# Optimization experiments

Hardware: AMD Instinct MI355X
Metric: run time of the kernel (lower is better)

The kernel has to match this reference:

```python
import jax, jax.numpy as jnp
import numpy as np

HEADS = 8
EMBED = 512


def setup_inputs() -> dict:
    key = jax.random.key(0)
    ks = jax.random.split(key, 9)
    N, KL, QL, S = 4, 512, 32, 64
    D = EMBED // HEADS
    return {
        "values": jax.random.normal(ks[0], (N, KL, EMBED), jnp.float32),
        "keys": jax.random.normal(ks[1], (N, KL, EMBED), jnp.float32),
        "query": jax.random.normal(ks[2], (N, QL, S, EMBED), jnp.float32),
        "mask": jax.random.randint(ks[3], (N, 1, 1, KL, 1), 0, 2, jnp.int32),
        "Wv": jax.random.normal(ks[4], (D, D), jnp.float32) * 0.05,
        "Wk": jax.random.normal(ks[5], (D, D), jnp.float32) * 0.05,
        "Wq": jax.random.normal(ks[6], (D, D), jnp.float32) * 0.05,
        "Wo": jax.random.normal(ks[7], (EMBED, EMBED), jnp.float32) * 0.05,
        "bo": jax.random.normal(ks[8], (EMBED,), jnp.float32) * 0.05,
    }


def reference(values, keys, query, mask, Wv, Wk, Wq, Wo, bo):
    N, KL, E = keys.shape
    QL, S = query.shape[1], query.shape[2]
    H = HEADS
    D = E // H
    # split heads, then per-head linear (weights shared across heads, torch y = x @ W.T)
    v = jnp.einsum('nkhd,ed->nkhe', values.reshape(N, KL, H, D), Wv)
    k = jnp.einsum('nkhd,ed->nkhe', keys.reshape(N, KL, H, D), Wk)
    q = jnp.einsum('nqshd,ed->nqshe', query.reshape(N, QL, S, H, D), Wq)
    # energy: [N, H, QL, KL, S]
    energy = jnp.einsum('nqshd,nkhd->nhqks', q, k)
    energy = jnp.where(mask == 0, jnp.float32(-1e20), energy)
    scale = jnp.float32(E ** 0.5)
    attention = jax.nn.softmax(energy / scale, axis=3)  # softmax over key axis
    out = jnp.einsum('nhqks,nkhd->nqshd', attention, v).reshape(N, QL, S, E)
    return out @ Wo.T + bo
```

## Files before the change

### kernel.cpp

```cpp
#include <hip/hip_runtime.h>
#include <math.h>


typedef __bf16 bf16;
typedef __attribute__((ext_vector_type(8))) __bf16 bf16x8;
typedef __attribute__((ext_vector_type(4))) __bf16 bf16x4;
typedef __attribute__((ext_vector_type(4))) float f32x4;

#define LW 68
#define LS 72
#define QSCALE (0.044194173824159216f * 1.4426950408889634f)
#define MASK_BIAS -64.0f

__device__ __forceinline__ bf16x8 cvt8(const float* p, float s) {
    float4 x0 = *(const float4*)p;
    float4 x1 = *(const float4*)(p + 4);
    return (bf16x8){(bf16)(x0.x * s), (bf16)(x0.y * s), (bf16)(x0.z * s), (bf16)(x0.w * s),
                    (bf16)(x1.x * s), (bf16)(x1.y * s), (bf16)(x1.z * s), (bf16)(x1.w * s)};
}

__global__ __launch_bounds__(256, 2) void kv_proj(const float* __restrict__ keys,
                                                  const float* __restrict__ values,
                                                  const float* __restrict__ Wk,
                                                  const float* __restrict__ Wv,
                                                  bf16* __restrict__ Kp,
                                                  bf16* __restrict__ Vt) {
    __shared__ bf16 Xk[32 * LW];
    __shared__ bf16 Xv[32 * LW];
    int t = threadIdx.x;
    int nh = blockIdx.x >> 4, klt = blockIdx.x & 15;
    int n = nh >> 3, h = nh & 7, kl0 = klt * 32;
    int w = t >> 6, quad = (t >> 4) & 3, c16 = t & 15;
#pragma unroll
    for (int i = 0; i < 2; ++i) {
        int f = t + i * 256, row = f >> 4, c4 = f & 15;
        float4 a = *(const float4*)(keys + ((long)n * 512 + kl0 + row) * 512 + h * 64 + c4 * 4);
        float4 b = *(const float4*)(values + ((long)n * 512 + kl0 + row) * 512 + h * 64 + c4 * 4);
        *(bf16x4*)&Xk[row * LW + c4 * 4] = (bf16x4){(bf16)a.x, (bf16)a.y, (bf16)a.z, (bf16)a.w};
        *(bf16x4*)&Xv[row * LW + c4 * 4] = (bf16x4){(bf16)b.x, (bf16)b.y, (bf16)b.z, (bf16)b.w};
    }
    __syncthreads();
    if (w < 2) {
        f32x4 acc[4];
#pragma unroll
        for (int nb = 0; nb < 4; ++nb) acc[nb] = (f32x4){0.f, 0.f, 0.f, 0.f};
#pragma unroll
        for (int kc = 0; kc < 2; ++kc) {
            bf16x8 a = *(const bf16x8*)&Xk[(16 * w + c16) * LW + 32 * kc + quad * 8];
#pragma unroll
            for (int nb = 0; nb < 4; ++nb) {
                bf16x8 b = cvt8(Wk + (16 * nb + c16) * 64 + 32 * kc + quad * 8, 1.0f);
                acc[nb] = __builtin_amdgcn_mfma_f32_16x16x32_bf16(a, b, acc[nb], 0, 0, 0);
            }
        }
#pragma unroll
        for (int nb = 0; nb < 4; ++nb)
#pragma unroll
            for (int r = 0; r < 4; ++r)
                Kp[((long)nh * 512 + kl0 + 16 * w + quad * 4 + r) * 64 + 16 * nb + c16] =
                    (bf16)acc[nb][r];
    } else {
        int w2 = w - 2;
        f32x4 acc[2][2];
#pragma unroll
        for (int mb = 0; mb < 2; ++mb)
#pragma unroll
            for (int nb = 0; nb < 2; ++nb) acc[mb][nb] = (f32x4){0.f, 0.f, 0.f, 0.f};
#pragma unroll
        for (int kc = 0; kc < 2; ++kc) {
#pragma unroll
            for (int mb = 0; mb < 2; ++mb) {
                bf16x8 a = cvt8(Wv + (32 * w2 + 16 * mb + c16) * 64 + 32 * kc + quad * 8, 1.0f);
#pragma unroll
                for (int nb = 0; nb < 2; ++nb) {
                    bf16x8 b = *(const bf16x8*)&Xv[(16 * nb + c16) * LW + 32 * kc + quad * 8];
                    acc[mb][nb] = __builtin_amdgcn_mfma_f32_16x16x32_bf16(a, b, acc[mb][nb], 0, 0, 0);
                }
            }
        }
#pragma unroll
        for (int mb = 0; mb < 2; ++mb)
#pragma unroll
            for (int nb = 0; nb < 2; ++nb)
#pragma unroll
                for (int r = 0; r < 4; ++r)
                    Vt[((long)nh * 64 + 32 * w2 + 16 * mb + quad * 4 + r) * 512 + kl0 + 16 * nb + c16] =
                        (bf16)acc[mb][nb][r];
    }
}

__global__ __launch_bounds__(256, 4) void attn(const float* __restrict__ query,
                                               const float* __restrict__ Wq,
                                               const bf16* __restrict__ Kp,
                                               const bf16* __restrict__ Vtg,
                                               const int* __restrict__ maskp,
                                               bf16* __restrict__ AOp,
                                               float* __restrict__ Lb) {
    __shared__ bf16 SX[64 * LS];
    __shared__ bf16 Kt[64 * LW];
    __shared__ bf16 Vs[64 * LW];
    int t = threadIdx.x;
    int nh = blockIdx.x & 31, half = (blockIdx.x >> 5) & 1, qtile = blockIdx.x >> 6;
    int n = nh >> 3, h = nh & 7;
    int r0 = qtile * 64;
    int kt0 = half * 4;
    int w = t >> 6, quad = (t >> 4) & 3, c16 = t & 15;
    const bf16* Kb = Kp + (long)nh * 512 * 64;
    const bf16* Vb = Vtg + (long)nh * 64 * 512;

    int prow0 = t >> 3, pcol0 = t & 7;
    int prow1 = (t + 256) >> 3, pcol1 = t & 7;
    bf16x8 pk0 = *(const bf16x8*)(Kb + (long)(kt0 * 64 + prow0) * 64 + pcol0 * 8);
    bf16x8 pk1 = *(const bf16x8*)(Kb + (long)(kt0 * 64 + prow1) * 64 + pcol1 * 8);
    bf16x8 pv0 = *(const bf16x8*)(Vb + (long)prow0 * 512 + kt0 * 64 + pcol0 * 8);
    bf16x8 pv1 = *(const bf16x8*)(Vb + (long)prow1 * 512 + kt0 * 64 + pcol1 * 8);

    bf16x8 wf[8];
#pragma unroll
    for (int nb = 0; nb < 4; ++nb)
#pragma unroll
        for (int kc = 0; kc < 2; ++kc)
            wf[nb * 2 + kc] = cvt8(Wq + (16 * nb + c16) * 64 + 32 * kc + quad * 8, QSCALE);

    {
        int l = t & 63;
        int rloc = 16 * w + (l >> 2);
        const float* qrow = query + ((long)n * 2048 + r0 + rloc) * 512 + h * 64;
#pragma unroll
        for (int j = 0; j < 4; ++j) {
            int c = (l & 3) + 4 * j;
            float4 a = *(const float4*)(qrow + c * 4);
            *(bf16x4*)&SX[rloc * LS + c * 4] = (bf16x4){(bf16)a.x, (bf16)a.y, (bf16)a.z, (bf16)a.w};
        }
    }
    f32x4 qa[4];
#pragma unroll
    for (int nb = 0; nb < 4; ++nb) qa[nb] = (f32x4){0.f, 0.f, 0.f, 0.f};
#pragma unroll
    for (int kc = 0; kc < 2; ++kc) {
        bf16x8 a = *(const bf16x8*)&SX[(16 * w + c16) * LS + 32 * kc + quad * 8];
#pragma unroll
        for (int nb = 0; nb < 4; ++nb)
            qa[nb] = __builtin_amdgcn_mfma_f32_16x16x32_bf16(a, wf[nb * 2 + kc], qa[nb], 0, 0, 0);
    }
#pragma unroll
    for (int nb = 0; nb < 4; ++nb)
#pragma unroll
        for (int r = 0; r < 4; ++r)
            SX[(16 * w + quad * 4 + r) * LS + 16 * nb + c16] = (bf16)qa[nb][r];
    bf16x8 qf[2];
#pragma unroll
    for (int kc = 0; kc < 2; ++kc)
        qf[kc] = *(const bf16x8*)&SX[(16 * w + c16) * LS + 32 * kc + quad * 8];

    f32x4 oacc[4];
#pragma unroll
    for (int mb = 0; mb < 4; ++mb) oacc[mb] = (f32x4){0.f, 0.f, 0.f, 0.f};
    float ps = 0.f;

    for (int kt = 0; kt < 4; ++kt) {
        int tk = kt0 + kt;
        if (kt) __syncthreads();
        *(bf16x8*)&Kt[prow0 * LW + pcol0 * 8] = pk0;
        *(bf16x8*)&Kt[prow1 * LW + pcol1 * 8] = pk1;
        *(bf16x8*)&Vs[prow0 * LW + pcol0 * 8] = pv0;
        *(bf16x8*)&Vs[prow1 * LW + pcol1 * 8] = pv1;
        __syncthreads();
        if (kt < 3) {
            pk0 = *(const bf16x8*)(Kb + (long)((tk + 1) * 64 + prow0) * 64 + pcol0 * 8);
            pk1 = *(const bf16x8*)(Kb + (long)((tk + 1) * 64 + prow1) * 64 + pcol1 * 8);
            pv0 = *(const bf16x8*)(Vb + (long)prow0 * 512 + (tk + 1) * 64 + pcol0 * 8);
            pv1 = *(const bf16x8*)(Vb + (long)prow1 * 512 + (tk + 1) * 64 + pcol1 * 8);
        }
        f32x4 sc[4];
#pragma unroll
        for (int mb = 0; mb < 4; ++mb) {
            int4 mk = *(const int4*)(maskp + n * 512 + tk * 64 + 16 * mb + quad * 4);
            sc[mb] = (f32x4){mk.x ? 0.f : MASK_BIAS, mk.y ? 0.f : MASK_BIAS,
                             mk.z ? 0.f : MASK_BIAS, mk.w ? 0.f : MASK_BIAS};
        }
#pragma unroll
        for (int kc = 0; kc < 2; ++kc) {
#pragma unroll
            for (int mb = 0; mb < 4; ++mb) {
                bf16x8 ka = *(const bf16x8*)&Kt[(16 * mb + c16) * LW + 32 * kc + quad * 8];
                sc[mb] = __builtin_amdgcn_mfma_f32_16x16x32_bf16(ka, qf[kc], sc[mb], 0, 0, 0);
            }
        }
#pragma unroll
        for (int mb = 0; mb < 4; ++mb) {
            float p0 = exp2f(sc[mb][0]);
            float p1 = exp2f(sc[mb][1]);
            float p2 = exp2f(sc[mb][2]);
            float p3 = exp2f(sc[mb][3]);
            ps += (p0 + p1) + (p2 + p3);
            *(bf16x4*)&SX[(16 * w + c16) * LS + 16 * mb + quad * 4] =
                (bf16x4){(bf16)p0, (bf16)p1, (bf16)p2, (bf16)p3};
        }
#pragma unroll
        for (int kc = 0; kc < 2; ++kc) {
            bf16x8 pb = *(const bf16x8*)&SX[(16 * w + c16) * LS + 32 * kc + quad * 8];
#pragma unroll
            for (int mb = 0; mb < 4; ++mb) {
                bf16x8 va = *(const bf16x8*)&Vs[(16 * mb + c16) * LW + 32 * kc + quad * 8];
                oacc[mb] = __builtin_amdgcn_mfma_f32_16x16x32_bf16(va, pb, oacc[mb], 0, 0, 0);
            }
        }
    }
    ps += __shfl_xor(ps, 16);
    ps += __shfl_xor(ps, 32);
    int row_g = r0 + 16 * w + c16;
    bf16* AO = AOp + (long)half * 4194304;
#pragma unroll
    for (int mb = 0; mb < 4; ++mb)
        *(bf16x4*)(AO + ((long)n * 2048 + row_g) * 512 + h * 64 + 16 * mb + quad * 4) =
            (bf16x4){(bf16)oacc[mb][0], (bf16)oacc[mb][1], (bf16)oacc[mb][2], (bf16)oacc[mb][3]};
    if (quad == 0) Lb[half * 65536 + nh * 2048 + row_g] = ps;
}

__global__ __launch_bounds__(256, 4) void out_gemm(const bf16* __restrict__ AOp,
                                                   const float* __restrict__ Lb,
                                                   const float* __restrict__ Wo,
                                                   const float* __restrict__ bo,
                                                   float* __restrict__ C) {
    __shared__ bf16 At[64 * LW];
    __shared__ bf16 Bt[64 * LW];
    int t = threadIdx.x;
    int br = blockIdx.x & 127, bc = blockIdx.x >> 7;
    int r0 = br * 64, c0 = bc * 64;
    int w = t >> 6, quad = (t >> 4) & 3, c16 = t & 15;
    const bf16* AO2 = AOp + 4194304;
    int arow[2], acol[2], wrow[4], wcol[4];
#pragma unroll
    for (int i = 0; i < 2; ++i) {
        int f = t + i * 256;
        arow[i] = f >> 3;
        acol[i] = f & 7;
    }
#pragma unroll
    for (int i = 0; i < 4; ++i) {
        int f = t + i * 256;
        wrow[i] = f >> 4;
        wcol[i] = f & 15;
    }
    bf16x8 pa1[2], pa2[2];
    float4 pw[4];
#pragma unroll
    for (int i = 0; i < 2; ++i) {
        pa1[i] = *(const bf16x8*)(AOp + (long)(r0 + arow[i]) * 512 + acol[i] * 8);
        pa2[i] = *(const bf16x8*)(AO2 + (long)(r0 + arow[i]) * 512 + acol[i] * 8);
    }
#pragma unroll
    for (int i = 0; i < 4; ++i)
        pw[i] = *(const float4*)(Wo + (long)(c0 + wrow[i]) * 512 + wcol[i] * 4);
    f32x4 acc[4];
#pragma unroll
    for (int nb = 0; nb < 4; ++nb) acc[nb] = (f32x4){0.f, 0.f, 0.f, 0.f};
    for (int k0 = 0; k0 < 512; k0 += 64) {
        int hh = k0 >> 6;
        if (k0) __syncthreads();
#pragma unroll
        for (int i = 0; i < 2; ++i) {
            int grow = r0 + arow[i];
            int lidx = ((grow >> 11) * 8 + hh) * 2048 + (grow & 2047);
            float il = 1.0f / (Lb[lidx] + Lb[65536 + lidx]);
            bf16x8 o;
#pragma unroll
            for (int e = 0; e < 8; ++e)
                o[e] = (bf16)(((float)pa1[i][e] + (float)pa2[i][e]) * il);
            *(bf16x8*)&At[arow[i] * LW + acol[i] * 8] = o;
        }
#pragma unroll
        for (int i = 0; i < 4; ++i)
            *(bf16x4*)&Bt[wrow[i] * LW + wcol[i] * 4] =
                (bf16x4){(bf16)pw[i].x, (bf16)pw[i].y, (bf16)pw[i].z, (bf16)pw[i].w};
        __syncthreads();
        if (k0 < 448) {
#pragma unroll
            for (int i = 0; i < 2; ++i) {
                pa1[i] = *(const bf16x8*)(AOp + (long)(r0 + arow[i]) * 512 + k0 + 64 + acol[i] * 8);
                pa2[i] = *(const bf16x8*)(AO2 + (long)(r0 + arow[i]) * 512 + k0 + 64 + acol[i] * 8);
            }
#pragma unroll
            for (int i = 0; i < 4; ++i)
                pw[i] = *(const float4*)(Wo + (long)(c0 + wrow[i]) * 512 + k0 + 64 + wcol[i] * 4);
        }
#pragma unroll
        for (int kc = 0; kc < 2; ++kc) {
            bf16x8 a = *(const bf16x8*)&At[(16 * w + c16) * LW + 32 * kc + quad * 8];
#pragma unroll
            for (int nb = 0; nb < 4; ++nb) {
                bf16x8 b = *(const bf16x8*)&Bt[(16 * nb + c16) * LW + 32 * kc + quad * 8];
                acc[nb] = __builtin_amdgcn_mfma_f32_16x16x32_bf16(a, b, acc[nb], 0, 0, 0);
            }
        }
    }
#pragma unroll
    for (int nb = 0; nb < 4; ++nb) {
        float bias = bo[c0 + 16 * nb + c16];
#pragma unroll
        for (int r = 0; r < 4; ++r)
            C[(long)(r0 + 16 * w + quad * 4 + r) * 512 + c0 + 16 * nb + c16] = acc[nb][r] + bias;
    }
}

extern "C" void kernel_launch(void* const* d_in, const int* in_sizes, int n_in,
                              void* d_out, int out_size, void* d_ws, size_t ws_size,
                              hipStream_t stream) {
    const float* values = (const float*)d_in[0];
    const float* keys   = (const float*)d_in[1];
    const float* query  = (const float*)d_in[2];
    const int*   maskp  = (const int*)d_in[3];
    const float* Wv     = (const float*)d_in[4];
    const float* Wk     = (const float*)d_in[5];
    const float* Wq     = (const float*)d_in[6];
    const float* Wo     = (const float*)d_in[7];
    const float* bo     = (const float*)d_in[8];
    float* out = (float*)d_out;

    bf16* ws = (bf16*)d_ws;
    bf16* Kp  = ws;
    bf16* Vt  = Kp + 1048576;
    bf16* AOp = Vt + 1048576;
    float* Lb = (float*)(AOp + 8388608);

    kv_proj<<<dim3(512), dim3(256), 0, stream>>>(keys, values, Wk, Wv, Kp, Vt);
    attn<<<dim3(2048), dim3(256), 0, stream>>>(query, Wq, Kp, Vt, maskp, AOp, Lb);
    out_gemm<<<dim3(1024), dim3(256), 0, stream>>>(AOp, Lb, Wo, bo, out);
}
```

Measured before the change: 144.2 us.

## Fuse attention with output projection, one 512-thread block per 16 rows

Merges the attention and output-GEMM kernels into a single kernel. Each 512-thread block handles 16 query rows across all 8 heads, one wave per head, and does not split the key length. The normalized attention output stays in shared memory and is multiplied directly by a bf16 copy of Wo, which the prep kernel now converts. This removes the global round-trip of the split partial outputs and row sums and one launch. In exchange, K and V fragments are read straight from global memory without LDS staging, and there are fewer, larger blocks.

New measurement: 187.2 us. 29.8% more time.

```diff
diff --git a/kernel.cpp b/kernel.cpp
--- a/kernel.cpp
+++ b/kernel.cpp
@@ -9,6 +9,7 @@
 
 #define LW 68
 #define LS 72
+#define AOW 524
 #define QSCALE (0.044194173824159216f * 1.4426950408889634f)
 #define MASK_BIAS -64.0f
 
@@ -19,15 +20,23 @@
                     (bf16)(x1.x * s), (bf16)(x1.y * s), (bf16)(x1.z * s), (bf16)(x1.w * s)};
 }
 
-__global__ __launch_bounds__(256, 2) void kv_proj(const float* __restrict__ keys,
-                                                  const float* __restrict__ values,
-                                                  const float* __restrict__ Wk,
-                                                  const float* __restrict__ Wv,
-                                                  bf16* __restrict__ Kp,
-                                                  bf16* __restrict__ Vt) {
+__global__ __launch_bounds__(256, 2) void prep(const float* __restrict__ keys,
+                                               const float* __restrict__ values,
+                                               const float* __restrict__ Wk,
+                                               const float* __restrict__ Wv,
+                                               const float* __restrict__ Wo,
+                                               bf16* __restrict__ Kp,
+                                               bf16* __restrict__ Vt,
+                                               bf16* __restrict__ Wo_bf) {
     __shared__ bf16 Xk[32 * LW];
     __shared__ bf16 Xv[32 * LW];
     int t = threadIdx.x;
+    if (blockIdx.x >= 512) {
+        int i0 = (blockIdx.x - 512) * 4096 + t * 16;
+        *(bf16x8*)(Wo_bf + i0) = cvt8(Wo + i0, 1.0f);
+        *(bf16x8*)(Wo_bf + i0 + 8) = cvt8(Wo + i0 + 8, 1.0f);
+        return;
+    }
     int nh = blockIdx.x >> 4, klt = blockIdx.x & 15;
     int n = nh >> 3, h = nh & 7, kl0 = klt * 32;
     int w = t >> 6, quad = (t >> 4) & 3, c16 = t & 15;
@@ -89,31 +98,24 @@
     }
 }
 
-__global__ __launch_bounds__(256, 4) void attn(const float* __restrict__ query,
-                                               const float* __restrict__ Wq,
-                                               const bf16* __restrict__ Kp,
-                                               const bf16* __restrict__ Vtg,
-                                               const int* __restrict__ maskp,
-                                               bf16* __restrict__ AOp,
-                                               float* __restrict__ Lb) {
-    __shared__ bf16 SX[64 * LS];
-    __shared__ bf16 Kt[64 * LW];
-    __shared__ bf16 Vs[64 * LW];
+__global__ __launch_bounds__(512, 4) void attn_gemm(const float* __restrict__ query,
+                                                    const float* __restrict__ Wq,
+                                                    const bf16* __restrict__ Kp,
+                                                    const bf16* __restrict__ Vtg,
+                                                    const int* __restrict__ maskp,
+                                                    const bf16* __restrict__ Wo_bf,
+                                                    const float* __restrict__ bo,
+                                                    float* __restrict__ out) {
+    __shared__ bf16 PW[128 * LS];
+    __shared__ bf16 AOt[16 * AOW];
     int t = threadIdx.x;
-    int nh = blockIdx.x & 31, half = (blockIdx.x >> 5) & 1, qtile = blockIdx.x >> 6;
-    int n = nh >> 3, h = nh & 7;
-    int r0 = qtile * 64;
-    int kt0 = half * 4;
     int w = t >> 6, quad = (t >> 4) & 3, c16 = t & 15;
+    int n = blockIdx.x >> 7, qt = blockIdx.x & 127;
+    int r0 = qt * 16;
+    int nh = n * 8 + w;
     const bf16* Kb = Kp + (long)nh * 512 * 64;
     const bf16* Vb = Vtg + (long)nh * 64 * 512;
-
-    int prow0 = t >> 3, pcol0 = t & 7;
-    int prow1 = (t + 256) >> 3, pcol1 = t & 7;
-    bf16x8 pk0 = *(const bf16x8*)(Kb + (long)(kt0 * 64 + prow0) * 64 + pcol0 * 8);
-    bf16x8 pk1 = *(const bf16x8*)(Kb + (long)(kt0 * 64 + prow1) * 64 + pcol1 * 8);
-    bf16x8 pv0 = *(const bf16x8*)(Vb + (long)prow0 * 512 + kt0 * 64 + pcol0 * 8);
-    bf16x8 pv1 = *(const bf16x8*)(Vb + (long)prow1 * 512 + kt0 * 64 + pcol1 * 8);
+    bf16* Pw = PW + w * 16 * LS;
 
     bf16x8 wf[8];
 #pragma unroll
@@ -124,13 +126,13 @@
 
     {
         int l = t & 63;
-        int rloc = 16 * w + (l >> 2);
-        const float* qrow = query + ((long)n * 2048 + r0 + rloc) * 512 + h * 64;
+        int rl = l >> 2;
+        const float* qrow = query + ((long)n * 2048 + r0 + rl) * 512 + w * 64;
 #pragma unroll
         for (int j = 0; j < 4; ++j) {
             int c = (l & 3) + 4 * j;
             float4 a = *(const float4*)(qrow + c * 4);
-            *(bf16x4*)&SX[rloc * LS + c * 4] = (bf16x4){(bf16)a.x, (bf16)a.y, (bf16)a.z, (bf16)a.w};
+            *(bf16x4*)&Pw[rl * LS + c * 4] = (bf16x4){(bf16)a.x, (bf16)a.y, (bf16)a.z, (bf16)a.w};
         }
     }
     f32x4 qa[4];
@@ -138,7 +140,7 @@
     for (int nb = 0; nb < 4; ++nb) qa[nb] = (f32x4){0.f, 0.f, 0.f, 0.f};
 #pragma unroll
     for (int kc = 0; kc < 2; ++kc) {
-        bf16x8 a = *(const bf16x8*)&SX[(16 * w + c16) * LS + 32 * kc + quad * 8];
+        bf16x8 a = *(const bf16x8*)&Pw[c16 * LS + 32 * kc + quad * 8];
 #pragma unroll
         for (int nb = 0; nb < 4; ++nb)
             qa[nb] = __builtin_amdgcn_mfma_f32_16x16x32_bf16(a, wf[nb * 2 + kc], qa[nb], 0, 0, 0);
@@ -147,35 +149,22 @@
     for (int nb = 0; nb < 4; ++nb)
 #pragma unroll
         for (int r = 0; r < 4; ++r)
-            SX[(16 * w + quad * 4 + r) * LS + 16 * nb + c16] = (bf16)qa[nb][r];
+            Pw[(quad * 4 + r) * LS + 16 * nb + c16] = (bf16)qa[nb][r];
     bf16x8 qf[2];
 #pragma unroll
     for (int kc = 0; kc < 2; ++kc)
-        qf[kc] = *(const bf16x8*)&SX[(16 * w + c16) * LS + 32 * kc + quad * 8];
+        qf[kc] = *(const bf16x8*)&Pw[c16 * LS + 32 * kc + quad * 8];
 
     f32x4 oacc[4];
 #pragma unroll
     for (int mb = 0; mb < 4; ++mb) oacc[mb] = (f32x4){0.f, 0.f, 0.f, 0.f};
     float ps = 0.f;
 
-    for (int kt = 0; kt < 4; ++kt) {
-        int tk = kt0 + kt;
-        if (kt) __syncthreads();
-        *(bf16x8*)&Kt[prow0 * LW + pcol0 * 8] = pk0;
-        *(bf16x8*)&Kt[prow1 * LW + pcol1 * 8] = pk1;
-        *(bf16x8*)&Vs[prow0 * LW + pcol0 * 8] = pv0;
-        *(bf16x8*)&Vs[prow1 * LW + pcol1 * 8] = pv1;
-        __syncthreads();
-        if (kt < 3) {
-            pk0 = *(const bf16x8*)(Kb + (long)((tk + 1) * 64 + prow0) * 64 + pcol0 * 8);
-            pk1 = *(const bf16x8*)(Kb + (long)((tk + 1) * 64 + prow1) * 64 + pcol1 * 8);
-            pv0 = *(const bf16x8*)(Vb + (long)prow0 * 512 + (tk + 1) * 64 + pcol0 * 8);
-            pv1 = *(const bf16x8*)(Vb + (long)prow1 * 512 + (tk + 1) * 64 + pcol1 * 8);
-        }
+    for (int kt = 0; kt < 8; ++kt) {
         f32x4 sc[4];
 #pragma unroll
         for (int mb = 0; mb < 4; ++mb) {
-            int4 mk = *(const int4*)(maskp + n * 512 + tk * 64 + 16 * mb + quad * 4);
+            int4 mk = *(const int4*)(maskp + n * 512 + kt * 64 + 16 * mb + quad * 4);
             sc[mb] = (f32x4){mk.x ? 0.f : MASK_BIAS, mk.y ? 0.f : MASK_BIAS,
                              mk.z ? 0.f : MASK_BIAS, mk.w ? 0.f : MASK_BIAS};
         }
@@ -183,7 +172,7 @@
         for (int kc = 0; kc < 2; ++kc) {
 #pragma unroll
             for (int mb = 0; mb < 4; ++mb) {
-                bf16x8 ka = *(const bf16x8*)&Kt[(16 * mb + c16) * LW + 32 * kc + quad * 8];
+                bf16x8 ka = *(const bf16x8*)(Kb + (long)(kt * 64 + 16 * mb + c16) * 64 + 32 * kc + quad * 8);
                 sc[mb] = __builtin_amdgcn_mfma_f32_16x16x32_bf16(ka, qf[kc], sc[mb], 0, 0, 0);
             }
         }
@@ -194,113 +183,48 @@
             float p2 = exp2f(sc[mb][2]);
             float p3 = exp2f(sc[mb][3]);
             ps += (p0 + p1) + (p2 + p3);
-            *(bf16x4*)&SX[(16 * w + c16) * LS + 16 * mb + quad * 4] =
+            *(bf16x4*)&Pw[c16 * LS + 16 * mb + quad * 4] =
                 (bf16x4){(bf16)p0, (bf16)p1, (bf16)p2, (bf16)p3};
         }
 #pragma unroll
         for (int kc = 0; kc < 2; ++kc) {
-            bf16x8 pb = *(const bf16x8*)&SX[(16 * w + c16) * LS + 32 * kc + quad * 8];
+            bf16x8 pb = *(const bf16x8*)&Pw[c16 * LS + 32 * kc + quad * 8];
 #pragma unroll
             for (int mb = 0; mb < 4; ++mb) {
-                bf16x8 va = *(const bf16x8*)&Vs[(16 * mb + c16) * LW + 32 * kc + quad * 8];
+                bf16x8 va = *(const bf16x8*)(Vb + (long)(16 * mb + c16) * 512 + kt * 64 + 32 * kc + quad * 8);
                 oacc[mb] = __builtin_amdgcn_mfma_f32_16x16x32_bf16(va, pb, oacc[mb], 0, 0, 0);
             }
         }
     }
     ps += __shfl_xor(ps, 16);
     ps += __shfl_xor(ps, 32);
-    int row_g = r0 + 16 * w + c16;
-    bf16* AO = AOp + (long)half * 4194304;
+    float il = 1.0f / ps;
 #pragma unroll
     for (int mb = 0; mb < 4; ++mb)
-        *(bf16x4*)(AO + ((long)n * 2048 + row_g) * 512 + h * 64 + 16 * mb + quad * 4) =
-            (bf16x4){(bf16)oacc[mb][0], (bf16)oacc[mb][1], (bf16)oacc[mb][2], (bf16)oacc[mb][3]};
-    if (quad == 0) Lb[half * 65536 + nh * 2048 + row_g] = ps;
-}
-
-__global__ __launch_bounds__(256, 4) void out_gemm(const bf16* __restrict__ AOp,
-                                                   const float* __restrict__ Lb,
-                                                   const float* __restrict__ Wo,
-                                                   const float* __restrict__ bo,
-                                                   float* __restrict__ C) {
-    __shared__ bf16 At[64 * LW];
-    __shared__ bf16 Bt[64 * LW];
-    int t = threadIdx.x;
-    int br = blockIdx.x & 127, bc = blockIdx.x >> 7;
-    int r0 = br * 64, c0 = bc * 64;
-    int w = t >> 6, quad = (t >> 4) & 3, c16 = t & 15;
-    const bf16* AO2 = AOp + 4194304;
-    int arow[2], acol[2], wrow[4], wcol[4];
-#pragma unroll
-    for (int i = 0; i < 2; ++i) {
-        int f = t + i * 256;
-        arow[i] = f >> 3;
-        acol[i] = f & 7;
-    }
-#pragma unroll
-    for (int i = 0; i < 4; ++i) {
-        int f = t + i * 256;
-        wrow[i] = f >> 4;
-        wcol[i] = f & 15;
-    }
-    bf16x8 pa1[2], pa2[2];
-    float4 pw[4];
-#pragma unroll
-    for (int i = 0; i < 2; ++i) {
-        pa1[i] = *(const bf16x8*)(AOp + (long)(r0 + arow[i]) * 512 + acol[i] * 8);
-        pa2[i] = *(const bf16x8*)(AO2 + (long)(r0 + arow[i]) * 512 + acol[i] * 8);
-    }
-#pragma unroll
-    for (int i = 0; i < 4; ++i)
-        pw[i] = *(const float4*)(Wo + (long)(c0 + wrow[i]) * 512 + wcol[i] * 4);
+        *(bf16x4*)&AOt[c16 * AOW + 64 * w + 16 * mb + quad * 4] =
+            (bf16x4){(bf16)(oacc[mb][0] * il), (bf16)(oacc[mb][1] * il),
+                     (bf16)(oacc[mb][2] * il), (bf16)(oacc[mb][3] * il)};
+    __syncthreads();
+
     f32x4 acc[4];
 #pragma unroll
     for (int nb = 0; nb < 4; ++nb) acc[nb] = (f32x4){0.f, 0.f, 0.f, 0.f};
-    for (int k0 = 0; k0 < 512; k0 += 64) {
-        int hh = k0 >> 6;
-        if (k0) __syncthreads();
-#pragma unroll
-        for (int i = 0; i < 2; ++i) {
-            int grow = r0 + arow[i];
-            int lidx = ((grow >> 11) * 8 + hh) * 2048 + (grow & 2047);
-            float il = 1.0f / (Lb[lidx] + Lb[65536 + lidx]);
-            bf16x8 o;
-#pragma unroll
-            for (int e = 0; e < 8; ++e)
-                o[e] = (bf16)(((float)pa1[i][e] + (float)pa2[i][e]) * il);
-            *(bf16x8*)&At[arow[i] * LW + acol[i] * 8] = o;
-        }
-#pragma unroll
-        for (int i = 0; i < 4; ++i)
-            *(bf16x4*)&Bt[wrow[i] * LW + wcol[i] * 4] =
-                (bf16x4){(bf16)pw[i].x, (bf16)pw[i].y, (bf16)pw[i].z, (bf16)pw[i].w};
-        __syncthreads();
-        if (k0 < 448) {
-#pragma unroll
-            for (int i = 0; i < 2; ++i) {
-                pa1[i] = *(const bf16x8*)(AOp + (long)(r0 + arow[i]) * 512 + k0 + 64 + acol[i] * 8);
-                pa2[i] = *(const bf16x8*)(AO2 + (long)(r0 + arow[i]) * 512 + k0 + 64 + acol[i] * 8);
-            }
-#pragma unroll
-            for (int i = 0; i < 4; ++i)
-                pw[i] = *(const float4*)(Wo + (long)(c0 + wrow[i]) * 512 + k0 + 64 + wcol[i] * 4);
-        }
-#pragma unroll
-        for (int kc = 0; kc < 2; ++kc) {
-            bf16x8 a = *(const bf16x8*)&At[(16 * w + c16) * LW + 32 * kc + quad * 8];
-#pragma unroll
-            for (int nb = 0; nb < 4; ++nb) {
-                bf16x8 b = *(const bf16x8*)&Bt[(16 * nb + c16) * LW + 32 * kc + quad * 8];
-                acc[nb] = __builtin_amdgcn_mfma_f32_16x16x32_bf16(a, b, acc[nb], 0, 0, 0);
-            }
+#pragma unroll
+    for (int ch = 0; ch < 16; ++ch) {
+        bf16x8 a = *(const bf16x8*)&AOt[c16 * AOW + 32 * ch + 8 * quad];
+#pragma unroll
+        for (int nb = 0; nb < 4; ++nb) {
+            bf16x8 b = *(const bf16x8*)(Wo_bf + (long)(64 * w + 16 * nb + c16) * 512 + 32 * ch + 8 * quad);
+            acc[nb] = __builtin_amdgcn_mfma_f32_16x16x32_bf16(a, b, acc[nb], 0, 0, 0);
         }
     }
 #pragma unroll
     for (int nb = 0; nb < 4; ++nb) {
-        float bias = bo[c0 + 16 * nb + c16];
+        float bias = bo[64 * w + 16 * nb + c16];
 #pragma unroll
         for (int r = 0; r < 4; ++r)
-            C[(long)(r0 + 16 * w + quad * 4 + r) * 512 + c0 + 16 * nb + c16] = acc[nb][r] + bias;
+            out[(long)(n * 2048 + r0 + quad * 4 + r) * 512 + 64 * w + 16 * nb + c16] =
+                acc[nb][r] + bias;
     }
 }
 
@@ -319,12 +243,10 @@
     float* out = (float*)d_out;
 
     bf16* ws = (bf16*)d_ws;
-    bf16* Kp  = ws;
-    bf16* Vt  = Kp + 1048576;
-    bf16* AOp = Vt + 1048576;
-    float* Lb = (float*)(AOp + 8388608);
-
-    kv_proj<<<dim3(512), dim3(256), 0, stream>>>(keys, values, Wk, Wv, Kp, Vt);
-    attn<<<dim3(2048), dim3(256), 0, stream>>>(query, Wq, Kp, Vt, maskp, AOp, Lb);
-    out_gemm<<<dim3(1024), dim3(256), 0, stream>>>(AOp, Lb, Wo, bo, out);
-}
+    bf16* Kp    = ws;
+    bf16* Vt    = Kp + 1048576;
+    bf16* Wo_bf = Vt + 1048576;
+
+    prep<<<dim3(576), dim3(256), 0, stream>>>(keys, values, Wk, Wv, Wo, Kp, Vt, Wo_bf);
+    attn_gemm<<<dim3(512), dim3(512), 0, stream>>>(query, Wq, Kp, Vt, maskp, Wo_bf, bo, out);
+}
```
